# Kernel optimization log

Measured on AMD Instinct MI355X. Metric: run time of the kernel, lower is better.

## Reference

```python
import jax, jax.numpy as jnp
import numpy as np

N, C, G = 262144, 256, 1024
R = C // 4  # reduction bottleneck


def _linear_w(key, out_dim, in_dim):
    # torch.nn.Linear default init: U(-1/sqrt(in), 1/sqrt(in)), weight shape [out, in]
    bound = 1.0 / np.sqrt(in_dim)
    return jax.random.uniform(key, (out_dim, in_dim), jnp.float32, -bound, bound)


def setup_inputs() -> dict:
    key = jax.random.key(0)
    ks = jax.random.split(key, 8)
    return {
        "x": jax.random.normal(ks[0], (N, C), jnp.float32),
        "glb_w1": _linear_w(ks[1], R, C),
        "glb_a": jnp.full((1,), 0.25, jnp.float32),   # PReLU param (default init 0.25)
        "glb_w2": _linear_w(ks[2], C, R),
        "local_w1": _linear_w(ks[3], R, C),
        "local_a": jnp.full((1,), 0.25, jnp.float32),
        "local_w2": _linear_w(ks[4], C, R),
        "attn_w1": _linear_w(ks[5], R, C),
        "attn_a": jnp.full((1,), 0.25, jnp.float32),
        "attn_w2": _linear_w(ks[6], C, R),
        "batch_idx": jnp.sort(jax.random.randint(ks[7], (N,), 0, G)),
        "num_graphs": G,
    }


def _mlp(h, w1, a, w2):
    # Linear(no bias) -> PReLU -> Linear(no bias)
    z = jnp.einsum('nc,rc->nr', h, w1)
    z = jnp.where(z >= 0, z, a * z)
    return jnp.einsum('nr,cr->nc', z, w2)


def reference(x, glb_w1, glb_a, glb_w2, local_w1, local_a, local_w2,
              attn_w1, attn_a, attn_w2, batch_idx, num_graphs):
    g = _mlp(x, glb_w1, glb_a, glb_w2)                                  # [N, C]
    seg_sum = jax.ops.segment_sum(g, batch_idx, num_segments=num_graphs)  # [G, C]
    cnt = jax.ops.segment_sum(jnp.ones((x.shape[0], 1), x.dtype), batch_idx,
                              num_segments=num_graphs)                  # [G, 1]
    seg_mean = seg_sum / jnp.maximum(cnt, 1.0)  # scatter_mean (0 for empty graphs)
    x_glb = seg_mean[batch_idx]                                          # gather back [N, C]
    loc = _mlp(x, local_w1, local_a, local_w2)                           # [N, C]
    attn = _mlp(loc + x_glb, attn_w1, attn_a, attn_w2)
    return jax.nn.sigmoid(attn)
```

## Files before the change

kernel.cpp:

```cpp
#include <hip/hip_runtime.h>

typedef unsigned short u16;
typedef __attribute__((ext_vector_type(8))) short short8;
typedef __attribute__((ext_vector_type(4))) float f32x4;
typedef __attribute__((ext_vector_type(4))) unsigned short u16x4;
typedef __attribute__((ext_vector_type(2))) unsigned u32x2;

#define NN 262144
#define CC 256
#define RR 64
#define GG 1024

#define SWZ(b, n) ((b) ^ (((n) & 7) << 4))


static __device__ __forceinline__ u16 f2bf(float f) {
  unsigned u = __builtin_bit_cast(unsigned, f);
  u += 0x7fffu + ((u >> 16) & 1u);
  return (u16)(u >> 16);
}

static __device__ __forceinline__ unsigned cvt_pk_bf16(float lo, float hi) {
  unsigned r;
  asm("v_cvt_pk_bf16_f32 %0, %1, %2" : "=v"(r) : "v"(lo), "v"(hi));
  return r;
}

static __device__ __forceinline__ void lgkm0() {
  __asm__ volatile("s_waitcnt lgkmcnt(0)" ::: "memory");
}

#define MFMA16(a, b, c) __builtin_amdgcn_mfma_f32_16x16x32_bf16((a), (b), (c), 0, 0, 0)

__global__ void k_cvt(const float* __restrict__ a0, const float* __restrict__ a1,
                      const float* __restrict__ a2, const float* __restrict__ a3,
                      const float* __restrict__ a4, const float* __restrict__ a5,
                      u16* __restrict__ dst) {
  int m = blockIdx.x >> 4;
  const float* s = (m == 0) ? a0 : (m == 1) ? a1 : (m == 2) ? a2
                 : (m == 3) ? a3 : (m == 4) ? a4 : a5;
  int off = (((blockIdx.x & 15) << 8) | threadIdx.x) << 2;
  f32x4 v = *(const f32x4*)(s + off);
  u16x4 p;
  p[0] = f2bf(v[0]); p[1] = f2bf(v[1]); p[2] = f2bf(v[2]); p[3] = f2bf(v[3]);
  *(u16x4*)(dst + m * 16384 + off) = p;
}


__global__ __launch_bounds__(256, 5) void k_glb(
    const float* __restrict__ x, const u16* __restrict__ wbf,
    const int* __restrict__ bidx, const float* __restrict__ pa,
    float* __restrict__ seg, int* __restrict__ cnt) {
  __shared__ __align__(16) char smem[32768];
  const int tid = threadIdx.x;
  const int wave = tid >> 6, lane = tid & 63;
  const int low = lane & 15, quad = lane >> 4;
  const int node0 = blockIdx.x << 6;
  const float alpha = pa[0];
  const u16* w1 = wbf;
  const u16* w2 = wbf + 16384;

  int myb_lb = (tid < 64) ? bidx[node0 + tid] : 0;

  const float* xsrc = x + (size_t)node0 * CC;
#pragma unroll
  for (int k = 0; k < 16; k++) {
    int f = k * 1024 + tid * 4;
    f32x4 v = *(const f32x4*)(xsrc + f);
    int node = f >> 8;
    u32x2 p;
    p[0] = cvt_pk_bf16(v[0], v[1]);
    p[1] = cvt_pk_bf16(v[2], v[3]);
    *(u32x2*)(smem + SWZ(node * 512 + (f & 255) * 2, node)) = p;
  }
  __syncthreads();

  f32x4 z[4] = {};
  const u16* w1p = w1 + (wave * 16 + low) * CC;
#pragma unroll
  for (int ks = 0; ks < 8; ks++) {
    short8 wa = *(const short8*)(w1p + ks * 32 + quad * 8);
#pragma unroll
    for (int nt = 0; nt < 4; nt++) {
      int node = nt * 16 + low;
      short8 xf = *(const short8*)(smem + SWZ(node * 512 + ks * 64 + quad * 16, node));
      z[nt] = MFMA16(wa, xf, z[nt]);
    }
  }
  __syncthreads();

  if (tid < 64) ((int*)(smem + 20480))[tid] = myb_lb;
#pragma unroll
  for (int nt = 0; nt < 4; nt++) {
    float v0 = z[nt][0], v1 = z[nt][1], v2 = z[nt][2], v3 = z[nt][3];
    v0 = v0 >= 0.f ? v0 : alpha * v0;
    v1 = v1 >= 0.f ? v1 : alpha * v1;
    v2 = v2 >= 0.f ? v2 : alpha * v2;
    v3 = v3 >= 0.f ? v3 : alpha * v3;
    int node = nt * 16 + low;
    u32x2 p;
    p[0] = cvt_pk_bf16(v0, v1);
    p[1] = cvt_pk_bf16(v2, v3);
    *(u32x2*)(smem + SWZ(node * 128 + wave * 32 + quad * 8, node)) = p;
  }
  __syncthreads();

  const int* lbp = (const int*)(smem + 20480);

  if (lane == 0) {
    int base = wave * 16;
    int cur = lbp[base], rl = 0;
#pragma unroll
    for (int n = 0; n < 16; n++) {
      int b = lbp[base + n];
      if (b != cur) { atomicAdd(cnt + cur, rl); rl = 0; cur = b; }
      rl++;
    }
    atomicAdd(cnt + cur, rl);
  }

  f32x4 g[4][4] = {};
#pragma unroll
  for (int ks2 = 0; ks2 < 2; ks2++) {
    short8 zf[4];
#pragma unroll
    for (int nt = 0; nt < 4; nt++) {
      int node = nt * 16 + low;
      zf[nt] = *(const short8*)(smem + SWZ(node * 128 + ks2 * 64 + quad * 16, node));
    }
#pragma unroll
    for (int mt = 0; mt < 4; mt++) {
      short8 wa = *(const short8*)(w2 + (wave * 64 + mt * 16 + low) * RR + ks2 * 32 + quad * 8);
#pragma unroll
      for (int nt = 0; nt < 4; nt++)
        g[nt][mt] = MFMA16(wa, zf[nt], g[nt][mt]);
    }
  }
  __syncthreads();

  float* slab = (float*)(smem + wave * 4352);
#pragma unroll
  for (int nt = 0; nt < 4; nt++) {
#pragma unroll
    for (int mt = 0; mt < 4; mt++)
      *(f32x4*)(slab + low * 68 + mt * 16 + quad * 4) = g[nt][mt];
    lgkm0();
    float acc = 0.f;
    int cur = lbp[nt * 16];
#pragma unroll
    for (int n = 0; n < 16; n++) {
      int b = lbp[nt * 16 + n];
      if (b != cur) {
        atomicAdd(seg + (size_t)cur * CC + wave * 64 + lane, acc);
        acc = 0.f; cur = b;
      }
      acc += slab[n * 68 + lane];
    }
    atomicAdd(seg + (size_t)cur * CC + wave * 64 + lane, acc);
    lgkm0();
  }
}

__global__ __launch_bounds__(256, 5) void k_attn(
    const float* __restrict__ x, const u16* __restrict__ wbf,
    const int* __restrict__ bidx, const float* __restrict__ seg,
    const int* __restrict__ cnt,
    const float* __restrict__ pal, const float* __restrict__ paa,
    float* __restrict__ out) {
  __shared__ __align__(16) char smem[32768];
  const int tid = threadIdx.x;
  const int wave = tid >> 6, lane = tid & 63;
  const int low = lane & 15, quad = lane >> 4;
  const int node0 = blockIdx.x << 6;
  const float al = pal[0], aa = paa[0];
  const u16* w1l = wbf + 2 * 16384;
  const u16* w2l = wbf + 3 * 16384;
  const u16* w1a = wbf + 4 * 16384;
  const u16* w2a = wbf + 5 * 16384;

  int bb[4];
#pragma unroll
  for (int nt = 0; nt < 4; nt++) bb[nt] = bidx[node0 + nt * 16 + low];
  int cc[4];
#pragma unroll
  for (int nt = 0; nt < 4; nt++) cc[nt] = cnt[bb[nt]];

  const float* xsrc = x + (size_t)node0 * CC;
#pragma unroll
  for (int k = 0; k < 16; k++) {
    int f = k * 1024 + tid * 4;
    f32x4 v = *(const f32x4*)(xsrc + f);
    int node = f >> 8;
    u32x2 p;
    p[0] = cvt_pk_bf16(v[0], v[1]);
    p[1] = cvt_pk_bf16(v[2], v[3]);
    *(u32x2*)(smem + SWZ(node * 512 + (f & 255) * 2, node)) = p;
  }
  __syncthreads();

  f32x4 z[4] = {};
  const u16* w1p = w1l + (wave * 16 + low) * CC;
#pragma unroll
  for (int ks = 0; ks < 8; ks++) {
    short8 wa = *(const short8*)(w1p + ks * 32 + quad * 8);
#pragma unroll
    for (int nt = 0; nt < 4; nt++) {
      int node = nt * 16 + low;
      short8 xf = *(const short8*)(smem + SWZ(node * 512 + ks * 64 + quad * 16, node));
      z[nt] = MFMA16(wa, xf, z[nt]);
    }
  }
  __syncthreads();
#pragma unroll
  for (int nt = 0; nt < 4; nt++) {
    float v0 = z[nt][0], v1 = z[nt][1], v2 = z[nt][2], v3 = z[nt][3];
    v0 = v0 >= 0.f ? v0 : al * v0;
    v1 = v1 >= 0.f ? v1 : al * v1;
    v2 = v2 >= 0.f ? v2 : al * v2;
    v3 = v3 >= 0.f ? v3 : al * v3;
    int node = nt * 16 + low;
    u32x2 p;
    p[0] = cvt_pk_bf16(v0, v1);
    p[1] = cvt_pk_bf16(v2, v3);
    *(u32x2*)(smem + SWZ(node * 128 + wave * 32 + quad * 8, node)) = p;
  }
  __syncthreads();

  f32x4 loc[4][4] = {};
#pragma unroll
  for (int ks2 = 0; ks2 < 2; ks2++) {
    short8 zf[4];
#pragma unroll
    for (int nt = 0; nt < 4; nt++) {
      int node = nt * 16 + low;
      zf[nt] = *(const short8*)(smem + SWZ(node * 128 + ks2 * 64 + quad * 16, node));
    }
#pragma unroll
    for (int mt = 0; mt < 4; mt++) {
      short8 wa = *(const short8*)(w2l + (wave * 64 + mt * 16 + low) * RR + ks2 * 32 + quad * 8);
#pragma unroll
      for (int nt = 0; nt < 4; nt++)
        loc[nt][mt] = MFMA16(wa, zf[nt], loc[nt][mt]);
    }
  }
  __syncthreads();

#pragma unroll
  for (int nt = 0; nt < 4; nt++) {
    const float* srow = seg + (size_t)bb[nt] * CC + wave * 64;
    float inv = (cc[nt] > 0) ? __builtin_amdgcn_rcpf((float)cc[nt]) : 0.0f;
    int node = nt * 16 + low;
#pragma unroll
    for (int mt = 0; mt < 4; mt++) {
      f32x4 sv = *(const f32x4*)(srow + mt * 16 + quad * 4);
      u32x2 p;
      p[0] = cvt_pk_bf16(fmaf(sv[0], inv, loc[nt][mt][0]),
                         fmaf(sv[1], inv, loc[nt][mt][1]));
      p[1] = cvt_pk_bf16(fmaf(sv[2], inv, loc[nt][mt][2]),
                         fmaf(sv[3], inv, loc[nt][mt][3]));
      *(u32x2*)(smem + SWZ(node * 512 + wave * 128 + mt * 32 + quad * 8, node)) = p;
    }
  }
  __syncthreads();

  f32x4 z2[4] = {};
  const u16* w1pa = w1a + (wave * 16 + low) * CC;
#pragma unroll
  for (int ks = 0; ks < 8; ks++) {
    short8 wa = *(const short8*)(w1pa + ks * 32 + quad * 8);
#pragma unroll
    for (int nt = 0; nt < 4; nt++) {
      int node = nt * 16 + low;
      short8 hf = *(const short8*)(smem + SWZ(node * 512 + ks * 64 + quad * 16, node));
      z2[nt] = MFMA16(wa, hf, z2[nt]);
    }
  }
  __syncthreads();
#pragma unroll
  for (int nt = 0; nt < 4; nt++) {
    float v0 = z2[nt][0], v1 = z2[nt][1], v2 = z2[nt][2], v3 = z2[nt][3];
    v0 = v0 >= 0.f ? v0 : aa * v0;
    v1 = v1 >= 0.f ? v1 : aa * v1;
    v2 = v2 >= 0.f ? v2 : aa * v2;
    v3 = v3 >= 0.f ? v3 : aa * v3;
    int node = nt * 16 + low;
    u32x2 p;
    p[0] = cvt_pk_bf16(v0, v1);
    p[1] = cvt_pk_bf16(v2, v3);
    *(u32x2*)(smem + SWZ(node * 128 + wave * 32 + quad * 8, node)) = p;
  }
  __syncthreads();

  f32x4 o[4][4] = {};
#pragma unroll
  for (int ks2 = 0; ks2 < 2; ks2++) {
    short8 zf[4];
#pragma unroll
    for (int nt = 0; nt < 4; nt++) {
      int node = nt * 16 + low;
      zf[nt] = *(const short8*)(smem + SWZ(node * 128 + ks2 * 64 + quad * 16, node));
    }
#pragma unroll
    for (int mt = 0; mt < 4; mt++) {
      short8 wa = *(const short8*)(w2a + (wave * 64 + mt * 16 + low) * RR + ks2 * 32 + quad * 8);
#pragma unroll
      for (int nt = 0; nt < 4; nt++)
        o[nt][mt] = MFMA16(wa, zf[nt], o[nt][mt]);
    }
  }
#pragma unroll
  for (int nt = 0; nt < 4; nt++)
#pragma unroll
    for (int mt = 0; mt < 4; mt++)
#pragma unroll
      for (int i = 0; i < 4; i++)
        o[nt][mt][i] = __builtin_amdgcn_rcpf(1.0f + __expf(-o[nt][mt][i]));
  __syncthreads();

  float* slab = (float*)(smem + wave * 4352);
#pragma unroll
  for (int nt = 0; nt < 4; nt++) {
#pragma unroll
    for (int mt = 0; mt < 4; mt++)
      *(f32x4*)(slab + low * 68 + mt * 16 + quad * 4) = o[nt][mt];
    lgkm0();
#pragma unroll
    for (int n = 0; n < 16; n++)
      out[(size_t)(node0 + nt * 16 + n) * CC + wave * 64 + lane] = slab[n * 68 + lane];
    lgkm0();
  }
}

extern "C" void kernel_launch(void* const* d_in, const int* in_sizes, int n_in,
                              void* d_out, int out_size, void* d_ws, size_t ws_size,
                              hipStream_t stream) {
  (void)in_sizes; (void)n_in; (void)out_size; (void)ws_size;
  const float* x   = (const float*)d_in[0];
  const float* w1g = (const float*)d_in[1];
  const float* ag  = (const float*)d_in[2];
  const float* w2g = (const float*)d_in[3];
  const float* w1l = (const float*)d_in[4];
  const float* al  = (const float*)d_in[5];
  const float* w2l = (const float*)d_in[6];
  const float* w1a = (const float*)d_in[7];
  const float* aa  = (const float*)d_in[8];
  const float* w2a = (const float*)d_in[9];
  const int* bidx  = (const int*)d_in[10];
  float* out = (float*)d_out;

  u16* wbf   = (u16*)d_ws;
  float* seg = (float*)((char*)d_ws + 196608);
  int* cnt   = (int*)((char*)d_ws + 196608 + 1048576);

  hipMemsetAsync(seg, 0, 1048576 + 4096, stream);
  k_cvt<<<96, 256, 0, stream>>>(w1g, w2g, w1l, w2l, w1a, w2a, wbf);
  k_glb<<<NN / 64, 256, 0, stream>>>(x, wbf, bidx, ag, seg, cnt);
  k_attn<<<NN / 64, 256, 0, stream>>>(x, wbf, bidx, seg, cnt, al, aa, out);
}
```

Measured before the change: 732.3 us.

## Stream second GEMM per node tile and relocate LDS buffers to drop barriers

Both kernels now compute the second linear layer one 16-node tile at a time and consume it immediately (segment atomics in k_glb, residual add and output store in k_attn), instead of keeping a 4x4 array of accumulators live. This shrinks accumulator register pressure. The occupancy hints move to amdgpu_waves_per_eu, set to 5 for k_glb and 4 for k_attn. In k_attn the bottleneck activations go to a separate LDS region at offset 32768, with LDS growing to 40 KB, so several __syncthreads barriers can be removed. The trade-offs are less MFMA batching per weight load, repeated w2 fragment loads per tile, and possibly lower occupancy for k_attn.

```diff
diff --git a/kernel.cpp b/kernel.cpp
--- a/kernel.cpp
+++ b/kernel.cpp
@@ -47,7 +47,8 @@
 }
 
 
-__global__ __launch_bounds__(256, 5) void k_glb(
+__global__ __launch_bounds__(256)
+__attribute__((amdgpu_waves_per_eu(5, 5))) void k_glb(
     const float* __restrict__ x, const u16* __restrict__ wbf,
     const int* __restrict__ bidx, const float* __restrict__ pa,
     float* __restrict__ seg, int* __restrict__ cnt) {
@@ -89,7 +90,7 @@
   }
   __syncthreads();
 
-  if (tid < 64) ((int*)(smem + 20480))[tid] = myb_lb;
+  if (tid < 64) ((int*)(smem + 25600))[tid] = myb_lb;
 #pragma unroll
   for (int nt = 0; nt < 4; nt++) {
     float v0 = z[nt][0], v1 = z[nt][1], v2 = z[nt][2], v3 = z[nt][3];
@@ -105,7 +106,7 @@
   }
   __syncthreads();
 
-  const int* lbp = (const int*)(smem + 20480);
+  const int* lbp = (const int*)(smem + 25600);
 
   if (lane == 0) {
     int base = wave * 16;
@@ -119,31 +120,23 @@
     atomicAdd(cnt + cur, rl);
   }
 
-  f32x4 g[4][4] = {};
-#pragma unroll
-  for (int ks2 = 0; ks2 < 2; ks2++) {
-    short8 zf[4];
-#pragma unroll
-    for (int nt = 0; nt < 4; nt++) {
-      int node = nt * 16 + low;
-      zf[nt] = *(const short8*)(smem + SWZ(node * 128 + ks2 * 64 + quad * 16, node));
-    }
-#pragma unroll
-    for (int mt = 0; mt < 4; mt++) {
-      short8 wa = *(const short8*)(w2 + (wave * 64 + mt * 16 + low) * RR + ks2 * 32 + quad * 8);
-#pragma unroll
-      for (int nt = 0; nt < 4; nt++)
-        g[nt][mt] = MFMA16(wa, zf[nt], g[nt][mt]);
-    }
-  }
-  __syncthreads();
-
-  float* slab = (float*)(smem + wave * 4352);
-#pragma unroll
-  for (int nt = 0; nt < 4; nt++) {
+  float* slab = (float*)(smem + 8192 + wave * 4352);
+#pragma unroll
+  for (int nt = 0; nt < 4; nt++) {
+    int node = nt * 16 + low;
+    f32x4 g[4] = {};
+#pragma unroll
+    for (int ks2 = 0; ks2 < 2; ks2++) {
+      short8 zf = *(const short8*)(smem + SWZ(node * 128 + ks2 * 64 + quad * 16, node));
+#pragma unroll
+      for (int mt = 0; mt < 4; mt++) {
+        short8 wa = *(const short8*)(w2 + (wave * 64 + mt * 16 + low) * RR + ks2 * 32 + quad * 8);
+        g[mt] = MFMA16(wa, zf, g[mt]);
+      }
+    }
 #pragma unroll
     for (int mt = 0; mt < 4; mt++)
-      *(f32x4*)(slab + low * 68 + mt * 16 + quad * 4) = g[nt][mt];
+      *(f32x4*)(slab + low * 68 + mt * 16 + quad * 4) = g[mt];
     lgkm0();
     float acc = 0.f;
     int cur = lbp[nt * 16];
@@ -161,13 +154,15 @@
   }
 }
 
-__global__ __launch_bounds__(256, 5) void k_attn(
+#define ZBOFF 32768
+__global__ __launch_bounds__(256)
+__attribute__((amdgpu_waves_per_eu(4, 4))) void k_attn(
     const float* __restrict__ x, const u16* __restrict__ wbf,
     const int* __restrict__ bidx, const float* __restrict__ seg,
     const int* __restrict__ cnt,
     const float* __restrict__ pal, const float* __restrict__ paa,
     float* __restrict__ out) {
-  __shared__ __align__(16) char smem[32768];
+  __shared__ __align__(16) char smem[40960];
   const int tid = threadIdx.x;
   const int wave = tid >> 6, lane = tid & 63;
   const int low = lane & 15, quad = lane >> 4;
@@ -210,7 +205,6 @@
       z[nt] = MFMA16(wa, xf, z[nt]);
     }
   }
-  __syncthreads();
 #pragma unroll
   for (int nt = 0; nt < 4; nt++) {
     float v0 = z[nt][0], v1 = z[nt][1], v2 = z[nt][2], v3 = z[nt][3];
@@ -222,42 +216,33 @@
     u32x2 p;
     p[0] = cvt_pk_bf16(v0, v1);
     p[1] = cvt_pk_bf16(v2, v3);
-    *(u32x2*)(smem + SWZ(node * 128 + wave * 32 + quad * 8, node)) = p;
-  }
-  __syncthreads();
-
-  f32x4 loc[4][4] = {};
-#pragma unroll
-  for (int ks2 = 0; ks2 < 2; ks2++) {
-    short8 zf[4];
-#pragma unroll
-    for (int nt = 0; nt < 4; nt++) {
-      int node = nt * 16 + low;
-      zf[nt] = *(const short8*)(smem + SWZ(node * 128 + ks2 * 64 + quad * 16, node));
-    }
-#pragma unroll
-    for (int mt = 0; mt < 4; mt++) {
-      short8 wa = *(const short8*)(w2l + (wave * 64 + mt * 16 + low) * RR + ks2 * 32 + quad * 8);
-#pragma unroll
-      for (int nt = 0; nt < 4; nt++)
-        loc[nt][mt] = MFMA16(wa, zf[nt], loc[nt][mt]);
-    }
-  }
-  __syncthreads();
-
-#pragma unroll
-  for (int nt = 0; nt < 4; nt++) {
+    *(u32x2*)(smem + ZBOFF + SWZ(node * 128 + wave * 32 + quad * 8, node)) = p;
+  }
+  __syncthreads();
+
+#pragma unroll
+  for (int nt = 0; nt < 4; nt++) {
+    int node = nt * 16 + low;
+    f32x4 loc[4] = {};
+#pragma unroll
+    for (int ks2 = 0; ks2 < 2; ks2++) {
+      short8 zf = *(const short8*)(smem + ZBOFF + SWZ(node * 128 + ks2 * 64 + quad * 16, node));
+#pragma unroll
+      for (int mt = 0; mt < 4; mt++) {
+        short8 wa = *(const short8*)(w2l + (wave * 64 + mt * 16 + low) * RR + ks2 * 32 + quad * 8);
+        loc[mt] = MFMA16(wa, zf, loc[mt]);
+      }
+    }
     const float* srow = seg + (size_t)bb[nt] * CC + wave * 64;
     float inv = (cc[nt] > 0) ? __builtin_amdgcn_rcpf((float)cc[nt]) : 0.0f;
-    int node = nt * 16 + low;
 #pragma unroll
     for (int mt = 0; mt < 4; mt++) {
       f32x4 sv = *(const f32x4*)(srow + mt * 16 + quad * 4);
       u32x2 p;
-      p[0] = cvt_pk_bf16(fmaf(sv[0], inv, loc[nt][mt][0]),
-                         fmaf(sv[1], inv, loc[nt][mt][1]));
-      p[1] = cvt_pk_bf16(fmaf(sv[2], inv, loc[nt][mt][2]),
-                         fmaf(sv[3], inv, loc[nt][mt][3]));
+      p[0] = cvt_pk_bf16(fmaf(sv[0], inv, loc[mt][0]),
+                         fmaf(sv[1], inv, loc[mt][1]));
+      p[1] = cvt_pk_bf16(fmaf(sv[2], inv, loc[mt][2]),
+                         fmaf(sv[3], inv, loc[mt][3]));
       *(u32x2*)(smem + SWZ(node * 512 + wave * 128 + mt * 32 + quad * 8, node)) = p;
     }
   }
@@ -275,7 +260,6 @@
       z2[nt] = MFMA16(wa, hf, z2[nt]);
     }
   }
-  __syncthreads();
 #pragma unroll
   for (int nt = 0; nt < 4; nt++) {
     float v0 = z2[nt][0], v1 = z2[nt][1], v2 = z2[nt][2], v3 = z2[nt][3];
@@ -287,42 +271,31 @@
     u32x2 p;
     p[0] = cvt_pk_bf16(v0, v1);
     p[1] = cvt_pk_bf16(v2, v3);
-    *(u32x2*)(smem + SWZ(node * 128 + wave * 32 + quad * 8, node)) = p;
-  }
-  __syncthreads();
-
-  f32x4 o[4][4] = {};
-#pragma unroll
-  for (int ks2 = 0; ks2 < 2; ks2++) {
-    short8 zf[4];
-#pragma unroll
-    for (int nt = 0; nt < 4; nt++) {
-      int node = nt * 16 + low;
-      zf[nt] = *(const short8*)(smem + SWZ(node * 128 + ks2 * 64 + quad * 16, node));
+    *(u32x2*)(smem + ZBOFF + SWZ(node * 128 + wave * 32 + quad * 8, node)) = p;
+  }
+  __syncthreads();
+
+  float* slab = (float*)(smem + wave * 4352);
+#pragma unroll
+  for (int nt = 0; nt < 4; nt++) {
+    int node = nt * 16 + low;
+    f32x4 o[4] = {};
+#pragma unroll
+    for (int ks2 = 0; ks2 < 2; ks2++) {
+      short8 zf = *(const short8*)(smem + ZBOFF + SWZ(node * 128 + ks2 * 64 + quad * 16, node));
+#pragma unroll
+      for (int mt = 0; mt < 4; mt++) {
+        short8 wa = *(const short8*)(w2a + (wave * 64 + mt * 16 + low) * RR + ks2 * 32 + quad * 8);
+        o[mt] = MFMA16(wa, zf, o[mt]);
+      }
     }
 #pragma unroll
     for (int mt = 0; mt < 4; mt++) {
-      short8 wa = *(const short8*)(w2a + (wave * 64 + mt * 16 + low) * RR + ks2 * 32 + quad * 8);
-#pragma unroll
-      for (int nt = 0; nt < 4; nt++)
-        o[nt][mt] = MFMA16(wa, zf[nt], o[nt][mt]);
-    }
-  }
-#pragma unroll
-  for (int nt = 0; nt < 4; nt++)
-#pragma unroll
-    for (int mt = 0; mt < 4; mt++)
 #pragma unroll
       for (int i = 0; i < 4; i++)
-        o[nt][mt][i] = __builtin_amdgcn_rcpf(1.0f + __expf(-o[nt][mt][i]));
-  __syncthreads();
-
-  float* slab = (float*)(smem + wave * 4352);
-#pragma unroll
-  for (int nt = 0; nt < 4; nt++) {
-#pragma unroll
-    for (int mt = 0; mt < 4; mt++)
-      *(f32x4*)(slab + low * 68 + mt * 16 + quad * 4) = o[nt][mt];
+        o[mt][i] = __builtin_amdgcn_rcpf(1.0f + __expf(-o[mt][i]));
+      *(f32x4*)(slab + low * 68 + mt * 16 + quad * 4) = o[mt];
+    }
     lgkm0();
 #pragma unroll
     for (int n = 0; n < 16; n++)
```

Result: faster. 666.2 us (-9.0%).
